# Kernel optimization log

Measured on AMD Instinct MI355X. Metric: run time of the kernel, lower is better.

Reference implementation:

```python
import jax, jax.numpy as jnp
import numpy as np

N_NODES = 50000
N_EDGES = 800000
D = 256


def setup_inputs() -> dict:
    key = jax.random.key(0)
    k1, k2, k3 = jax.random.split(key, 3)
    node_features = jax.random.normal(k1, (N_NODES, D), dtype=jnp.float32)
    edge_index = jax.random.randint(k2, (2, N_EDGES), 0, N_NODES, dtype=jnp.int64)
    # GCNConv linear weight (glorot-ish scale) and bias
    W = jax.random.normal(k3, (D, D), dtype=jnp.float32) * (1.0 / np.sqrt(D))
    b = jnp.zeros((D,), dtype=jnp.float32)
    alpha = jnp.full((1,), 0.5, dtype=jnp.float32)
    return {"node_features": node_features, "edge_index": edge_index, "W": W, "b": b, "alpha": alpha}


def _gcn_conv(x, edge_index, W, b):
    # PyG GCNConv: add self-loops, symmetric deg^{-1/2} normalization,
    # x' = W x, out[i] = sum_{j in N(i)} norm_ij * x'_j + b
    N = x.shape[0]
    loop = jnp.arange(N, dtype=edge_index.dtype)
    src = jnp.concatenate([edge_index[0], loop])  # [E+N]
    dst = jnp.concatenate([edge_index[1], loop])
    deg = jax.ops.segment_sum(jnp.ones(src.shape, dtype=x.dtype), dst, num_segments=N)
    dinv = jnp.where(deg > 0, jax.lax.rsqrt(jnp.maximum(deg, 1.0)), 0.0)
    norm = dinv[src] * dinv[dst]  # [E+N]
    h = x @ W.T  # [N, D]
    msg = h[src] * norm[:, None]  # gather + scale
    out = jax.ops.segment_sum(msg, dst, num_segments=N)  # scatter-add to targets
    return out + b


def reference(node_features, edge_index, W, b, alpha):
    updated = _gcn_conv(node_features, edge_index, W, b)
    a = alpha[0]
    # eval mode: dropout = identity; alpha-weighted residual blend
    return a * node_features + (1.0 - a) * updated
```

## Files before the change

### kernel.cpp

```cpp
#include <hip/hip_runtime.h>

#define N_NODES 50000
#define N_EDGES 800000
#define D 256
#define SLOT 64
#define GEMM_BLOCKS 391
#define FILL_BLOCKS 1563

typedef unsigned short bf16_t;
typedef __attribute__((ext_vector_type(8))) short short8;
typedef __attribute__((ext_vector_type(8))) unsigned short ushort8_t;
typedef __attribute__((ext_vector_type(4))) float f32x4;

__device__ inline float b2f(bf16_t u) {
    union { float f; unsigned v; } t; t.v = ((unsigned)u) << 16; return t.f;
}
__device__ inline bf16_t f2b(float f) {
    union { float f; unsigned v; } t; t.f = f;
    unsigned u = t.v;
    return (bf16_t)((u + 0x7FFFu + ((u >> 16) & 1u)) >> 16);
}
__device__ inline unsigned cvt_pk_bf16(float lo, float hi) {
    unsigned r;
    asm("v_cvt_pk_bf16_f32 %0, %1, %2" : "=v"(r) : "v"(lo), "v"(hi));
    return r;
}
__device__ inline short8 cvt8(float4 a, float4 b) {
    union { short8 s; unsigned u[4]; } t;
    t.u[0] = cvt_pk_bf16(a.x, a.y);
    t.u[1] = cvt_pk_bf16(a.z, a.w);
    t.u[2] = cvt_pk_bf16(b.x, b.y);
    t.u[3] = cvt_pk_bf16(b.z, b.w);
    return t.s;
}

__global__ void initcur_kernel(int* __restrict__ cursor) {
    int i = blockIdx.x * 256 + threadIdx.x;
    if (i < N_NODES) cursor[i] = i << 6;
}

__global__ __launch_bounds__(512) void k1_kernel(const float* __restrict__ x,
                                                 const float* __restrict__ W,
                                                 bf16_t* __restrict__ h,
                                                 const int* __restrict__ ei,
                                                 int* __restrict__ cursor,
                                                 int* __restrict__ csr_src) {
    __shared__ __align__(16) bf16_t As[128 * 32];
    __shared__ __align__(16) bf16_t Bs[256 * 32];

    const int tid = threadIdx.x;

    if (blockIdx.x >= GEMM_BLOCKS) {
        int e = (blockIdx.x - GEMM_BLOCKS) * 512 + tid;
        if (e < N_EDGES) {
            int s = ei[e];
            int d = ei[N_EDGES + e];
            if ((unsigned)d < (unsigned)N_NODES) {
                int pos = atomicAdd(&cursor[d], 1);
                csr_src[pos] = s;
            }
        }
        return;
    }

    const int wid  = tid >> 6;
    const int lane = tid & 63;
    const int wr = wid >> 2;
    const int wc = wid & 3;
    const int row0 = blockIdx.x * 128;
    const int lr = lane & 15;
    const int lk = (lane >> 4) * 8;

    const int srow = tid >> 2;
    const int sq   = tid & 3;
    int sr = row0 + srow;
    if (sr >= N_NODES) sr = N_NODES - 1;
    const float* agp = &x[(size_t)sr * D + sq * 8];
    bf16_t* alp = &As[srow * 32 + sq * 8];

    float4 areg[16];
#pragma unroll
    for (int s = 0; s < 8; s++) {
        const float4* p = reinterpret_cast<const float4*>(&agp[s * 32]);
        areg[2 * s]     = p[0];
        areg[2 * s + 1] = p[1];
    }

    f32x4 acc[4][4] = {};

#pragma unroll
    for (int s = 0; s < 8; s++) {
        *reinterpret_cast<short8*>(alp) = cvt8(areg[2 * s], areg[2 * s + 1]);
#pragma unroll
        for (int j = 0; j < 2; j++) {
            int brow = (j * 512 + tid) >> 2;
            const float4* q = reinterpret_cast<const float4*>(&W[(size_t)brow * D + s * 32 + sq * 8]);
            float4 w0 = q[0], w1 = q[1];
            *reinterpret_cast<short8*>(&Bs[brow * 32 + sq * 8]) = cvt8(w0, w1);
        }
        __syncthreads();

        short8 a[4], b[4];
#pragma unroll
        for (int m = 0; m < 4; m++)
            a[m] = *reinterpret_cast<const short8*>(&As[(wr * 64 + m * 16 + lr) * 32 + lk]);
#pragma unroll
        for (int n = 0; n < 4; n++)
            b[n] = *reinterpret_cast<const short8*>(&Bs[(wc * 64 + n * 16 + lr) * 32 + lk]);
#pragma unroll
        for (int m = 0; m < 4; m++)
#pragma unroll
            for (int n = 0; n < 4; n++)
                acc[m][n] = __builtin_amdgcn_mfma_f32_16x16x32_bf16(a[m], b[n], acc[m][n], 0, 0, 0);
        __syncthreads();
    }

#pragma unroll
    for (int m = 0; m < 4; m++) {
        int rbase = row0 + wr * 64 + m * 16 + (lane >> 4) * 4;
#pragma unroll
        for (int j = 0; j < 4; j++) {
            int rr = rbase + j;
            if (rr < N_NODES) {
#pragma unroll
                for (int n = 0; n < 4; n++)
                    h[(size_t)rr * D + wc * 64 + n * 16 + lr] = f2b(acc[m][n][j]);
            }
        }
    }
}

__global__ void dinv_kernel(const int* __restrict__ cursor, float* __restrict__ dinv) {
    int i = blockIdx.x * 256 + threadIdx.x;
    if (i < N_NODES) {
        int cnt = cursor[i] - (i << 6);
        dinv[i] = rsqrtf((float)(cnt + 1));
    }
}

__global__ __launch_bounds__(256) void gather_kernel(const int* __restrict__ cursor,
                                                     const int* __restrict__ csr_src,
                                                     const float* __restrict__ dinv,
                                                     const bf16_t* __restrict__ h,
                                                     const float* __restrict__ x,
                                                     const float* __restrict__ b,
                                                     const float* __restrict__ alpha,
                                                     float* __restrict__ out) {
    const int half = (threadIdx.x >> 5) & 1;
    const int wv   = threadIdx.x >> 6;
    const int ln   = threadIdx.x & 31;
    const int n = blockIdx.x * 8 + wv * 2 + half;
    if (n >= N_NODES) return;
    const int col = ln * 8;

    const int beg = n << 6;
    const int end = cursor[n];
    const float dn = dinv[n];
    const bf16_t* hl = h + col;

    float a0 = 0.f, a1 = 0.f, a2 = 0.f, a3 = 0.f,
          a4 = 0.f, a5 = 0.f, a6 = 0.f, a7 = 0.f;
    int k = beg;
    for (; k + 3 < end; k += 4) {
        int s0 = csr_src[k], s1 = csr_src[k + 1], s2 = csr_src[k + 2], s3 = csr_src[k + 3];
        float n0 = dinv[s0] * dn, n1 = dinv[s1] * dn, n2 = dinv[s2] * dn, n3 = dinv[s3] * dn;
        ushort8_t r0 = *reinterpret_cast<const ushort8_t*>(&hl[(size_t)s0 * D]);
        ushort8_t r1 = *reinterpret_cast<const ushort8_t*>(&hl[(size_t)s1 * D]);
        ushort8_t r2 = *reinterpret_cast<const ushort8_t*>(&hl[(size_t)s2 * D]);
        ushort8_t r3 = *reinterpret_cast<const ushort8_t*>(&hl[(size_t)s3 * D]);
        a0 += b2f(r0[0]) * n0 + b2f(r1[0]) * n1 + b2f(r2[0]) * n2 + b2f(r3[0]) * n3;
        a1 += b2f(r0[1]) * n0 + b2f(r1[1]) * n1 + b2f(r2[1]) * n2 + b2f(r3[1]) * n3;
        a2 += b2f(r0[2]) * n0 + b2f(r1[2]) * n1 + b2f(r2[2]) * n2 + b2f(r3[2]) * n3;
        a3 += b2f(r0[3]) * n0 + b2f(r1[3]) * n1 + b2f(r2[3]) * n2 + b2f(r3[3]) * n3;
        a4 += b2f(r0[4]) * n0 + b2f(r1[4]) * n1 + b2f(r2[4]) * n2 + b2f(r3[4]) * n3;
        a5 += b2f(r0[5]) * n0 + b2f(r1[5]) * n1 + b2f(r2[5]) * n2 + b2f(r3[5]) * n3;
        a6 += b2f(r0[6]) * n0 + b2f(r1[6]) * n1 + b2f(r2[6]) * n2 + b2f(r3[6]) * n3;
        a7 += b2f(r0[7]) * n0 + b2f(r1[7]) * n1 + b2f(r2[7]) * n2 + b2f(r3[7]) * n3;
    }
    for (; k < end; k++) {
        int s0 = csr_src[k];
        float n0 = dinv[s0] * dn;
        ushort8_t r0 = *reinterpret_cast<const ushort8_t*>(&hl[(size_t)s0 * D]);
        a0 += b2f(r0[0]) * n0; a1 += b2f(r0[1]) * n0;
        a2 += b2f(r0[2]) * n0; a3 += b2f(r0[3]) * n0;
        a4 += b2f(r0[4]) * n0; a5 += b2f(r0[5]) * n0;
        a6 += b2f(r0[6]) * n0; a7 += b2f(r0[7]) * n0;
    }

    const float dv2 = dn * dn;
    const float a   = alpha[0];
    ushort8_t hv = *reinterpret_cast<const ushort8_t*>(&hl[(size_t)n * D]);
    const float4* xp = reinterpret_cast<const float4*>(&x[(size_t)n * D + col]);
    const float4* bp = reinterpret_cast<const float4*>(&b[col]);
    float4 xv0 = xp[0], xv1 = xp[1];
    float4 bv0 = bp[0], bv1 = bp[1];
    float4 r0, r1;
    r0.x = a * xv0.x + (1.0f - a) * (a0 + dv2 * b2f(hv[0]) + bv0.x);
    r0.y = a * xv0.y + (1.0f - a) * (a1 + dv2 * b2f(hv[1]) + bv0.y);
    r0.z = a * xv0.z + (1.0f - a) * (a2 + dv2 * b2f(hv[2]) + bv0.z);
    r0.w = a * xv0.w + (1.0f - a) * (a3 + dv2 * b2f(hv[3]) + bv0.w);
    r1.x = a * xv1.x + (1.0f - a) * (a4 + dv2 * b2f(hv[4]) + bv1.x);
    r1.y = a * xv1.y + (1.0f - a) * (a5 + dv2 * b2f(hv[5]) + bv1.y);
    r1.z = a * xv1.z + (1.0f - a) * (a6 + dv2 * b2f(hv[6]) + bv1.z);
    r1.w = a * xv1.w + (1.0f - a) * (a7 + dv2 * b2f(hv[7]) + bv1.w);
    float4* op = reinterpret_cast<float4*>(&out[(size_t)n * D + col]);
    op[0] = r0;
    op[1] = r1;
}

extern "C" void kernel_launch(void* const* d_in, const int* in_sizes, int n_in,
                              void* d_out, int out_size, void* d_ws, size_t ws_size,
                              hipStream_t stream) {
    const float* x     = (const float*)d_in[0];
    const int*   ei    = (const int*)d_in[1];
    const float* W     = (const float*)d_in[2];
    const float* b     = (const float*)d_in[3];
    const float* alpha = (const float*)d_in[4];
    float* out = (float*)d_out;

    char* ws = (char*)d_ws;
    const size_t HB = (size_t)N_NODES * D * 2;
    bf16_t* h      = (bf16_t*)ws;
    int*   cursor  = (int*)  (ws + HB);
    float* dinv    = (float*)(ws + HB + 200000);
    int*   csr_src = (int*)  (ws + HB + 400000);

    initcur_kernel<<<(N_NODES + 255) / 256, 256, 0, stream>>>(cursor);
    k1_kernel<<<GEMM_BLOCKS + FILL_BLOCKS, 512, 0, stream>>>(x, W, h, ei, cursor, csr_src);
    dinv_kernel<<<(N_NODES + 255) / 256, 256, 0, stream>>>(cursor, dinv);
    gather_kernel<<<(N_NODES + 7) / 8, 256, 0, stream>>>(cursor, csr_src, dinv, h, x, b, alpha, out);
}
```

Measured before the change: 157.2 us.

## Stage full W in swizzled LDS, double-buffer A, fold CSR fill into GEMM blocks

The GEMM kernel now converts and stores all of W into LDS once, in an XOR-swizzled layout, instead of reloading a 32-wide slice on every k-step. The A tile is double-buffered, so each k-step needs one barrier instead of two. The separate edge-fill blocks are removed: each GEMM block handles 2048 edges of the CSR scatter while its x loads are in flight. The trade-off is about 144KB of LDS per block, which limits each CU to one block and leaves less latency hiding for the 391 blocks.

After: 140.9 us. -10.4%, faster.

```diff
diff --git a/kernel.cpp b/kernel.cpp
--- a/kernel.cpp
+++ b/kernel.cpp
@@ -5,7 +5,6 @@
 #define D 256
 #define SLOT 64
 #define GEMM_BLOCKS 391
-#define FILL_BLOCKS 1563
 
 typedef unsigned short bf16_t;
 typedef __attribute__((ext_vector_type(8))) short short8;
@@ -45,39 +44,17 @@
                                                  const int* __restrict__ ei,
                                                  int* __restrict__ cursor,
                                                  int* __restrict__ csr_src) {
-    __shared__ __align__(16) bf16_t As[128 * 32];
-    __shared__ __align__(16) bf16_t Bs[256 * 32];
+    __shared__ __align__(16) bf16_t Bs[256 * 256];
+    __shared__ __align__(16) bf16_t As[2 * 128 * 32];
 
     const int tid = threadIdx.x;
-
-    if (blockIdx.x >= GEMM_BLOCKS) {
-        int e = (blockIdx.x - GEMM_BLOCKS) * 512 + tid;
-        if (e < N_EDGES) {
-            int s = ei[e];
-            int d = ei[N_EDGES + e];
-            if ((unsigned)d < (unsigned)N_NODES) {
-                int pos = atomicAdd(&cursor[d], 1);
-                csr_src[pos] = s;
-            }
-        }
-        return;
-    }
-
-    const int wid  = tid >> 6;
-    const int lane = tid & 63;
-    const int wr = wid >> 2;
-    const int wc = wid & 3;
     const int row0 = blockIdx.x * 128;
-    const int lr = lane & 15;
-    const int lk = (lane >> 4) * 8;
 
     const int srow = tid >> 2;
     const int sq   = tid & 3;
     int sr = row0 + srow;
     if (sr >= N_NODES) sr = N_NODES - 1;
     const float* agp = &x[(size_t)sr * D + sq * 8];
-    bf16_t* alp = &As[srow * 32 + sq * 8];
-
     float4 areg[16];
 #pragma unroll
     for (int s = 0; s < 8; s++) {
@@ -86,38 +63,79 @@
         areg[2 * s + 1] = p[1];
     }
 
+    {
+        int e0 = blockIdx.x * 2048 + tid;
+        int ss[4], pos[4];
+        bool ok[4];
+#pragma unroll
+        for (int j = 0; j < 4; j++) {
+            int e = e0 + j * 512;
+            ok[j] = (e < N_EDGES);
+            int s = 0, d = 0;
+            if (ok[j]) { s = ei[e]; d = ei[N_EDGES + e]; }
+            ss[j] = s;
+            if (ok[j] && (unsigned)d < (unsigned)N_NODES)
+                pos[j] = atomicAdd(&cursor[d], 1);
+            else
+                ok[j] = false;
+        }
+#pragma unroll
+        for (int j = 0; j < 4; j++)
+            if (ok[j]) csr_src[pos[j]] = ss[j];
+    }
+
+#pragma unroll
+    for (int it = 0; it < 16; it++) {
+        int idx = it * 512 + tid;
+        int col = idx >> 5;
+        int c   = idx & 31;
+        const float4* q = reinterpret_cast<const float4*>(&W[(size_t)col * D + c * 8]);
+        short8 wv = cvt8(q[0], q[1]);
+        int phys = c ^ (col & 7);
+        *reinterpret_cast<short8*>(&Bs[col * 256 + (phys << 3)]) = wv;
+    }
+    __syncthreads();
+
+    const int wid  = tid >> 6;
+    const int lane = tid & 63;
+    const int wr = wid >> 2;
+    const int wc = wid & 3;
+    const int lr = lane & 15;
+    const int g  = lane >> 4;
+
     f32x4 acc[4][4] = {};
 
 #pragma unroll
     for (int s = 0; s < 8; s++) {
-        *reinterpret_cast<short8*>(alp) = cvt8(areg[2 * s], areg[2 * s + 1]);
-#pragma unroll
-        for (int j = 0; j < 2; j++) {
-            int brow = (j * 512 + tid) >> 2;
-            const float4* q = reinterpret_cast<const float4*>(&W[(size_t)brow * D + s * 32 + sq * 8]);
-            float4 w0 = q[0], w1 = q[1];
-            *reinterpret_cast<short8*>(&Bs[brow * 32 + sq * 8]) = cvt8(w0, w1);
-        }
+        *reinterpret_cast<short8*>(
+            &As[(s & 1) * 4096 + srow * 32 + ((sq ^ (srow & 3)) << 3)]) =
+            cvt8(areg[2 * s], areg[2 * s + 1]);
         __syncthreads();
 
         short8 a[4], b[4];
 #pragma unroll
-        for (int m = 0; m < 4; m++)
-            a[m] = *reinterpret_cast<const short8*>(&As[(wr * 64 + m * 16 + lr) * 32 + lk]);
-#pragma unroll
-        for (int n = 0; n < 4; n++)
-            b[n] = *reinterpret_cast<const short8*>(&Bs[(wc * 64 + n * 16 + lr) * 32 + lk]);
+        for (int m = 0; m < 4; m++) {
+            int row = wr * 64 + m * 16 + lr;
+            a[m] = *reinterpret_cast<const short8*>(
+                &As[(s & 1) * 4096 + row * 32 + ((g ^ (row & 3)) << 3)]);
+        }
+#pragma unroll
+        for (int n = 0; n < 4; n++) {
+            int col = wc * 64 + n * 16 + lr;
+            int c   = s * 4 + g;
+            int phys = c ^ (col & 7);
+            b[n] = *reinterpret_cast<const short8*>(&Bs[col * 256 + (phys << 3)]);
+        }
 #pragma unroll
         for (int m = 0; m < 4; m++)
 #pragma unroll
             for (int n = 0; n < 4; n++)
                 acc[m][n] = __builtin_amdgcn_mfma_f32_16x16x32_bf16(a[m], b[n], acc[m][n], 0, 0, 0);
-        __syncthreads();
     }
 
 #pragma unroll
     for (int m = 0; m < 4; m++) {
-        int rbase = row0 + wr * 64 + m * 16 + (lane >> 4) * 4;
+        int rbase = row0 + wr * 64 + m * 16 + g * 4;
 #pragma unroll
         for (int j = 0; j < 4; j++) {
             int rr = rbase + j;
@@ -226,7 +244,7 @@
     int*   csr_src = (int*)  (ws + HB + 400000);
 
     initcur_kernel<<<(N_NODES + 255) / 256, 256, 0, stream>>>(cursor);
-    k1_kernel<<<GEMM_BLOCKS + FILL_BLOCKS, 512, 0, stream>>>(x, W, h, ei, cursor, csr_src);
+    k1_kernel<<<GEMM_BLOCKS, 512, 0, stream>>>(x, W, h, ei, cursor, csr_src);
     dinv_kernel<<<(N_NODES + 255) / 256, 256, 0, stream>>>(cursor, dinv);
     gather_kernel<<<(N_NODES + 7) / 8, 256, 0, stream>>>(cursor, csr_src, dinv, h, x, b, alpha, out);
 }
```

## Aggregate raw bf16 features first, then fuse the GEMM into the gather kernel

Applied to the files above, without the earlier changes.

Uses linearity to reorder the computation as (A·x)·Wᵀ instead of A·(x·Wᵀ). Node features are converted to bf16 in a prep kernel, gathered and normalized per node, staged in shared memory, then multiplied by bf16 W with MFMA inside the same kernel before the residual blend. This removes the separate GEMM pass and its intermediate h write and read. In exchange, every block re-reads all of W from global or cache, the aggregated sums are rounded to bf16 before the matmul, and the edge-fill work now shares a launch with the conversion work.

After: 166.3 us. 5.8% more time.

```diff
diff --git a/kernel.cpp b/kernel.cpp
--- a/kernel.cpp
+++ b/kernel.cpp
@@ -4,8 +4,10 @@
 #define N_EDGES 800000
 #define D 256
 #define SLOT 64
-#define GEMM_BLOCKS 391
-#define FILL_BLOCKS 1563
+#define PADK 280
+#define FILL_BLOCKS 196
+#define CVTX_BLOCKS 3125
+#define CVTW_BLOCKS 16
 
 typedef unsigned short bf16_t;
 typedef __attribute__((ext_vector_type(8))) short short8;
@@ -14,11 +16,6 @@
 
 __device__ inline float b2f(bf16_t u) {
     union { float f; unsigned v; } t; t.v = ((unsigned)u) << 16; return t.f;
-}
-__device__ inline bf16_t f2b(float f) {
-    union { float f; unsigned v; } t; t.f = f;
-    unsigned u = t.v;
-    return (bf16_t)((u + 0x7FFFu + ((u >> 16) & 1u)) >> 16);
 }
 __device__ inline unsigned cvt_pk_bf16(float lo, float hi) {
     unsigned r;
@@ -39,94 +36,40 @@
     if (i < N_NODES) cursor[i] = i << 6;
 }
 
-__global__ __launch_bounds__(512) void k1_kernel(const float* __restrict__ x,
-                                                 const float* __restrict__ W,
-                                                 bf16_t* __restrict__ h,
-                                                 const int* __restrict__ ei,
-                                                 int* __restrict__ cursor,
-                                                 int* __restrict__ csr_src) {
-    __shared__ __align__(16) bf16_t As[128 * 32];
-    __shared__ __align__(16) bf16_t Bs[256 * 32];
-
+__global__ __launch_bounds__(512) void prep_kernel(const float* __restrict__ x,
+                                                   const float* __restrict__ W,
+                                                   const int* __restrict__ ei,
+                                                   int* __restrict__ cursor,
+                                                   int* __restrict__ csr_src,
+                                                   bf16_t* __restrict__ xb,
+                                                   bf16_t* __restrict__ Wb) {
     const int tid = threadIdx.x;
-
-    if (blockIdx.x >= GEMM_BLOCKS) {
-        int e = (blockIdx.x - GEMM_BLOCKS) * 512 + tid;
-        if (e < N_EDGES) {
-            int s = ei[e];
-            int d = ei[N_EDGES + e];
-            if ((unsigned)d < (unsigned)N_NODES) {
-                int pos = atomicAdd(&cursor[d], 1);
-                csr_src[pos] = s;
+    const int bid = blockIdx.x;
+
+    if (bid < FILL_BLOCKS) {
+        int e0 = bid * 4096 + tid;
+#pragma unroll
+        for (int j = 0; j < 8; j++) {
+            int e = e0 + j * 512;
+            if (e < N_EDGES) {
+                int s = ei[e];
+                int d = ei[N_EDGES + e];
+                if ((unsigned)d < (unsigned)N_NODES) {
+                    int pos = atomicAdd(&cursor[d], 1);
+                    csr_src[pos] = s;
+                }
             }
         }
-        return;
-    }
-
-    const int wid  = tid >> 6;
-    const int lane = tid & 63;
-    const int wr = wid >> 2;
-    const int wc = wid & 3;
-    const int row0 = blockIdx.x * 128;
-    const int lr = lane & 15;
-    const int lk = (lane >> 4) * 8;
-
-    const int srow = tid >> 2;
-    const int sq   = tid & 3;
-    int sr = row0 + srow;
-    if (sr >= N_NODES) sr = N_NODES - 1;
-    const float* agp = &x[(size_t)sr * D + sq * 8];
-    bf16_t* alp = &As[srow * 32 + sq * 8];
-
-    float4 areg[16];
-#pragma unroll
-    for (int s = 0; s < 8; s++) {
-        const float4* p = reinterpret_cast<const float4*>(&agp[s * 32]);
-        areg[2 * s]     = p[0];
-        areg[2 * s + 1] = p[1];
-    }
-
-    f32x4 acc[4][4] = {};
-
-#pragma unroll
-    for (int s = 0; s < 8; s++) {
-        *reinterpret_cast<short8*>(alp) = cvt8(areg[2 * s], areg[2 * s + 1]);
-#pragma unroll
-        for (int j = 0; j < 2; j++) {
-            int brow = (j * 512 + tid) >> 2;
-            const float4* q = reinterpret_cast<const float4*>(&W[(size_t)brow * D + s * 32 + sq * 8]);
-            float4 w0 = q[0], w1 = q[1];
-            *reinterpret_cast<short8*>(&Bs[brow * 32 + sq * 8]) = cvt8(w0, w1);
-        }
-        __syncthreads();
-
-        short8 a[4], b[4];
-#pragma unroll
-        for (int m = 0; m < 4; m++)
-            a[m] = *reinterpret_cast<const short8*>(&As[(wr * 64 + m * 16 + lr) * 32 + lk]);
-#pragma unroll
-        for (int n = 0; n < 4; n++)
-            b[n] = *reinterpret_cast<const short8*>(&Bs[(wc * 64 + n * 16 + lr) * 32 + lk]);
-#pragma unroll
-        for (int m = 0; m < 4; m++)
-#pragma unroll
-            for (int n = 0; n < 4; n++)
-                acc[m][n] = __builtin_amdgcn_mfma_f32_16x16x32_bf16(a[m], b[n], acc[m][n], 0, 0, 0);
-        __syncthreads();
-    }
-
-#pragma unroll
-    for (int m = 0; m < 4; m++) {
-        int rbase = row0 + wr * 64 + m * 16 + (lane >> 4) * 4;
-#pragma unroll
-        for (int j = 0; j < 4; j++) {
-            int rr = rbase + j;
-            if (rr < N_NODES) {
-#pragma unroll
-                for (int n = 0; n < 4; n++)
-                    h[(size_t)rr * D + wc * 64 + n * 16 + lr] = f2b(acc[m][n][j]);
-            }
-        }
+    } else if (bid < FILL_BLOCKS + CVTX_BLOCKS) {
+        int i = (bid - FILL_BLOCKS) * 512 + tid;
+        const float4* p = reinterpret_cast<const float4*>(x) + (size_t)i * 2;
+        float4 v0 = p[0], v1 = p[1];
+        *reinterpret_cast<short8*>(&xb[(size_t)i * 8]) = cvt8(v0, v1);
+    } else {
+        int i = (bid - FILL_BLOCKS - CVTX_BLOCKS) * 512 + tid;
+        const float4* p = reinterpret_cast<const float4*>(W) + (size_t)i * 2;
+        float4 v0 = p[0], v1 = p[1];
+        *reinterpret_cast<short8*>(&Wb[(size_t)i * 8]) = cvt8(v0, v1);
     }
 }
 
@@ -138,74 +81,102 @@
     }
 }
 
-__global__ __launch_bounds__(256) void gather_kernel(const int* __restrict__ cursor,
-                                                     const int* __restrict__ csr_src,
-                                                     const float* __restrict__ dinv,
-                                                     const bf16_t* __restrict__ h,
-                                                     const float* __restrict__ x,
-                                                     const float* __restrict__ b,
-                                                     const float* __restrict__ alpha,
-                                                     float* __restrict__ out) {
-    const int half = (threadIdx.x >> 5) & 1;
-    const int wv   = threadIdx.x >> 6;
-    const int ln   = threadIdx.x & 31;
-    const int n = blockIdx.x * 8 + wv * 2 + half;
-    if (n >= N_NODES) return;
+__global__ __launch_bounds__(512) void gather_gemm_kernel(const int* __restrict__ cursor,
+                                                          const int* __restrict__ csr_src,
+                                                          const float* __restrict__ dinv,
+                                                          const bf16_t* __restrict__ xb,
+                                                          const bf16_t* __restrict__ Wb,
+                                                          const float* __restrict__ x,
+                                                          const float* __restrict__ b,
+                                                          const float* __restrict__ alpha,
+                                                          float* __restrict__ out) {
+    __shared__ __align__(16) bf16_t As[16 * PADK];
+
+    const int tid = threadIdx.x;
+    const int r   = tid >> 5;
+    const int ln  = tid & 31;
+    const int n   = blockIdx.x * 16 + r;
     const int col = ln * 8;
 
-    const int beg = n << 6;
-    const int end = cursor[n];
-    const float dn = dinv[n];
-    const bf16_t* hl = h + col;
-
-    float a0 = 0.f, a1 = 0.f, a2 = 0.f, a3 = 0.f,
-          a4 = 0.f, a5 = 0.f, a6 = 0.f, a7 = 0.f;
-    int k = beg;
-    for (; k + 3 < end; k += 4) {
-        int s0 = csr_src[k], s1 = csr_src[k + 1], s2 = csr_src[k + 2], s3 = csr_src[k + 3];
-        float n0 = dinv[s0] * dn, n1 = dinv[s1] * dn, n2 = dinv[s2] * dn, n3 = dinv[s3] * dn;
-        ushort8_t r0 = *reinterpret_cast<const ushort8_t*>(&hl[(size_t)s0 * D]);
-        ushort8_t r1 = *reinterpret_cast<const ushort8_t*>(&hl[(size_t)s1 * D]);
-        ushort8_t r2 = *reinterpret_cast<const ushort8_t*>(&hl[(size_t)s2 * D]);
-        ushort8_t r3 = *reinterpret_cast<const ushort8_t*>(&hl[(size_t)s3 * D]);
-        a0 += b2f(r0[0]) * n0 + b2f(r1[0]) * n1 + b2f(r2[0]) * n2 + b2f(r3[0]) * n3;
-        a1 += b2f(r0[1]) * n0 + b2f(r1[1]) * n1 + b2f(r2[1]) * n2 + b2f(r3[1]) * n3;
-        a2 += b2f(r0[2]) * n0 + b2f(r1[2]) * n1 + b2f(r2[2]) * n2 + b2f(r3[2]) * n3;
-        a3 += b2f(r0[3]) * n0 + b2f(r1[3]) * n1 + b2f(r2[3]) * n2 + b2f(r3[3]) * n3;
-        a4 += b2f(r0[4]) * n0 + b2f(r1[4]) * n1 + b2f(r2[4]) * n2 + b2f(r3[4]) * n3;
-        a5 += b2f(r0[5]) * n0 + b2f(r1[5]) * n1 + b2f(r2[5]) * n2 + b2f(r3[5]) * n3;
-        a6 += b2f(r0[6]) * n0 + b2f(r1[6]) * n1 + b2f(r2[6]) * n2 + b2f(r3[6]) * n3;
-        a7 += b2f(r0[7]) * n0 + b2f(r1[7]) * n1 + b2f(r2[7]) * n2 + b2f(r3[7]) * n3;
-    }
-    for (; k < end; k++) {
-        int s0 = csr_src[k];
-        float n0 = dinv[s0] * dn;
-        ushort8_t r0 = *reinterpret_cast<const ushort8_t*>(&hl[(size_t)s0 * D]);
-        a0 += b2f(r0[0]) * n0; a1 += b2f(r0[1]) * n0;
-        a2 += b2f(r0[2]) * n0; a3 += b2f(r0[3]) * n0;
-        a4 += b2f(r0[4]) * n0; a5 += b2f(r0[5]) * n0;
-        a6 += b2f(r0[6]) * n0; a7 += b2f(r0[7]) * n0;
-    }
-
-    const float dv2 = dn * dn;
-    const float a   = alpha[0];
-    ushort8_t hv = *reinterpret_cast<const ushort8_t*>(&hl[(size_t)n * D]);
-    const float4* xp = reinterpret_cast<const float4*>(&x[(size_t)n * D + col]);
-    const float4* bp = reinterpret_cast<const float4*>(&b[col]);
-    float4 xv0 = xp[0], xv1 = xp[1];
-    float4 bv0 = bp[0], bv1 = bp[1];
-    float4 r0, r1;
-    r0.x = a * xv0.x + (1.0f - a) * (a0 + dv2 * b2f(hv[0]) + bv0.x);
-    r0.y = a * xv0.y + (1.0f - a) * (a1 + dv2 * b2f(hv[1]) + bv0.y);
-    r0.z = a * xv0.z + (1.0f - a) * (a2 + dv2 * b2f(hv[2]) + bv0.z);
-    r0.w = a * xv0.w + (1.0f - a) * (a3 + dv2 * b2f(hv[3]) + bv0.w);
-    r1.x = a * xv1.x + (1.0f - a) * (a4 + dv2 * b2f(hv[4]) + bv1.x);
-    r1.y = a * xv1.y + (1.0f - a) * (a5 + dv2 * b2f(hv[5]) + bv1.y);
-    r1.z = a * xv1.z + (1.0f - a) * (a6 + dv2 * b2f(hv[6]) + bv1.z);
-    r1.w = a * xv1.w + (1.0f - a) * (a7 + dv2 * b2f(hv[7]) + bv1.w);
-    float4* op = reinterpret_cast<float4*>(&out[(size_t)n * D + col]);
-    op[0] = r0;
-    op[1] = r1;
+    {
+        const int beg = n << 6;
+        const int end = cursor[n];
+        const float dn = dinv[n];
+        const bf16_t* hl = xb + col;
+
+        float a0 = 0.f, a1 = 0.f, a2 = 0.f, a3 = 0.f,
+              a4 = 0.f, a5 = 0.f, a6 = 0.f, a7 = 0.f;
+        int k = beg;
+        for (; k + 3 < end; k += 4) {
+            int s0 = csr_src[k], s1 = csr_src[k + 1], s2 = csr_src[k + 2], s3 = csr_src[k + 3];
+            float n0 = dinv[s0] * dn, n1 = dinv[s1] * dn, n2 = dinv[s2] * dn, n3 = dinv[s3] * dn;
+            ushort8_t r0 = *reinterpret_cast<const ushort8_t*>(&hl[(size_t)s0 * D]);
+            ushort8_t r1 = *reinterpret_cast<const ushort8_t*>(&hl[(size_t)s1 * D]);
+            ushort8_t r2 = *reinterpret_cast<const ushort8_t*>(&hl[(size_t)s2 * D]);
+            ushort8_t r3 = *reinterpret_cast<const ushort8_t*>(&hl[(size_t)s3 * D]);
+            a0 += b2f(r0[0]) * n0 + b2f(r1[0]) * n1 + b2f(r2[0]) * n2 + b2f(r3[0]) * n3;
+            a1 += b2f(r0[1]) * n0 + b2f(r1[1]) * n1 + b2f(r2[1]) * n2 + b2f(r3[1]) * n3;
+            a2 += b2f(r0[2]) * n0 + b2f(r1[2]) * n1 + b2f(r2[2]) * n2 + b2f(r3[2]) * n3;
+            a3 += b2f(r0[3]) * n0 + b2f(r1[3]) * n1 + b2f(r2[3]) * n2 + b2f(r3[3]) * n3;
+            a4 += b2f(r0[4]) * n0 + b2f(r1[4]) * n1 + b2f(r2[4]) * n2 + b2f(r3[4]) * n3;
+            a5 += b2f(r0[5]) * n0 + b2f(r1[5]) * n1 + b2f(r2[5]) * n2 + b2f(r3[5]) * n3;
+            a6 += b2f(r0[6]) * n0 + b2f(r1[6]) * n1 + b2f(r2[6]) * n2 + b2f(r3[6]) * n3;
+            a7 += b2f(r0[7]) * n0 + b2f(r1[7]) * n1 + b2f(r2[7]) * n2 + b2f(r3[7]) * n3;
+        }
+        for (; k < end; k++) {
+            int s0 = csr_src[k];
+            float n0 = dinv[s0] * dn;
+            ushort8_t r0 = *reinterpret_cast<const ushort8_t*>(&hl[(size_t)s0 * D]);
+            a0 += b2f(r0[0]) * n0; a1 += b2f(r0[1]) * n0;
+            a2 += b2f(r0[2]) * n0; a3 += b2f(r0[3]) * n0;
+            a4 += b2f(r0[4]) * n0; a5 += b2f(r0[5]) * n0;
+            a6 += b2f(r0[6]) * n0; a7 += b2f(r0[7]) * n0;
+        }
+        const float dv2 = dn * dn;
+        ushort8_t hv = *reinterpret_cast<const ushort8_t*>(&hl[(size_t)n * D]);
+        a0 += dv2 * b2f(hv[0]); a1 += dv2 * b2f(hv[1]);
+        a2 += dv2 * b2f(hv[2]); a3 += dv2 * b2f(hv[3]);
+        a4 += dv2 * b2f(hv[4]); a5 += dv2 * b2f(hv[5]);
+        a6 += dv2 * b2f(hv[6]); a7 += dv2 * b2f(hv[7]);
+
+        union { short8 s; unsigned u[4]; } t;
+        t.u[0] = cvt_pk_bf16(a0, a1);
+        t.u[1] = cvt_pk_bf16(a2, a3);
+        t.u[2] = cvt_pk_bf16(a4, a5);
+        t.u[3] = cvt_pk_bf16(a6, a7);
+        *reinterpret_cast<short8*>(&As[r * PADK + col]) = t.s;
+    }
+    __syncthreads();
+
+    const int w    = tid >> 6;
+    const int lane = tid & 63;
+    const int lr = lane & 15;
+    const int g  = lane >> 4;
+
+    f32x4 acc0 = {}, acc1 = {};
+    const bf16_t* wp0 = &Wb[(size_t)(w * 32 + lr) * D];
+    const bf16_t* wp1 = &Wb[(size_t)(w * 32 + 16 + lr) * D];
+#pragma unroll
+    for (int ks = 0; ks < 8; ks++) {
+        short8 a = *reinterpret_cast<const short8*>(&As[lr * PADK + ks * 32 + g * 8]);
+        short8 b0 = *reinterpret_cast<const short8*>(&wp0[ks * 32 + g * 8]);
+        short8 b1 = *reinterpret_cast<const short8*>(&wp1[ks * 32 + g * 8]);
+        acc0 = __builtin_amdgcn_mfma_f32_16x16x32_bf16(a, b0, acc0, 0, 0, 0);
+        acc1 = __builtin_amdgcn_mfma_f32_16x16x32_bf16(a, b1, acc1, 0, 0, 0);
+    }
+
+    const float av = alpha[0];
+    const int c0 = w * 32 + lr;
+    const int c1 = c0 + 16;
+    const float b0v = b[c0];
+    const float b1v = b[c1];
+#pragma unroll
+    for (int j = 0; j < 4; j++) {
+        int node = blockIdx.x * 16 + g * 4 + j;
+        size_t base = (size_t)node * D;
+        out[base + c0] = av * x[base + c0] + (1.0f - av) * (acc0[j] + b0v);
+        out[base + c1] = av * x[base + c1] + (1.0f - av) * (acc1[j] + b1v);
+    }
 }
 
 extern "C" void kernel_launch(void* const* d_in, const int* in_sizes, int n_in,
@@ -219,14 +190,17 @@
     float* out = (float*)d_out;
 
     char* ws = (char*)d_ws;
-    const size_t HB = (size_t)N_NODES * D * 2;
-    bf16_t* h      = (bf16_t*)ws;
-    int*   cursor  = (int*)  (ws + HB);
-    float* dinv    = (float*)(ws + HB + 200000);
-    int*   csr_src = (int*)  (ws + HB + 400000);
+    const size_t XB = (size_t)N_NODES * D * 2;
+    bf16_t* xb     = (bf16_t*)ws;
+    bf16_t* Wb     = (bf16_t*)(ws + XB);
+    int*   cursor  = (int*)  (ws + XB + 131072);
+    float* dinv    = (float*)(ws + XB + 331072);
+    int*   csr_src = (int*)  (ws + XB + 531072);
 
     initcur_kernel<<<(N_NODES + 255) / 256, 256, 0, stream>>>(cursor);
-    k1_kernel<<<GEMM_BLOCKS + FILL_BLOCKS, 512, 0, stream>>>(x, W, h, ei, cursor, csr_src);
+    prep_kernel<<<FILL_BLOCKS + CVTX_BLOCKS + CVTW_BLOCKS, 512, 0, stream>>>(
+        x, W, ei, cursor, csr_src, xb, Wb);
     dinv_kernel<<<(N_NODES + 255) / 256, 256, 0, stream>>>(cursor, dinv);
-    gather_kernel<<<(N_NODES + 7) / 8, 256, 0, stream>>>(cursor, csr_src, dinv, h, x, b, alpha, out);
-}
+    gather_gemm_kernel<<<N_NODES / 16, 512, 0, stream>>>(
+        cursor, csr_src, dinv, xb, Wb, x, b, alpha, out);
+}
```

## Use 8-way striped CSR slots with sentinel padding and precast W to bf16

Applied to the files above, without the earlier changes.

Each node's adjacency slot grows to 128 entries and is split into 8 interleaved cursors chosen by edge index. This spreads atomic contention across sub-counters, and the gather can read rows of 8 source indices with int4 loads. Unused slots are pre-filled with a sentinel node whose h row and dinv are zero, so the gather loop runs a branch-free 8-wide unrolled body up to the longest stripe. W is converted to bf16 once in an init kernel rather than by every GEMM block, and fill blocks each process 8 edges. In exchange the init kernel writes a 25.6 MB sentinel buffer, and the gather wastes reads whenever stripes are uneven.

Result: slower. 164.0 us (+4.3%).

```diff
diff --git a/kernel.cpp b/kernel.cpp
--- a/kernel.cpp
+++ b/kernel.cpp
@@ -3,9 +3,12 @@
 #define N_NODES 50000
 #define N_EDGES 800000
 #define D 256
-#define SLOT 64
+#define SLOT 128
 #define GEMM_BLOCKS 391
-#define FILL_BLOCKS 1563
+#define FILL_BLOCKS 196
+#define CUR_INIT_BLOCKS 1563
+#define SENT_BLOCKS 6250
+#define WCVT_BLOCKS 32
 
 typedef unsigned short bf16_t;
 typedef __attribute__((ext_vector_type(8))) short short8;
@@ -34,13 +37,42 @@
     return t.s;
 }
 
-__global__ void initcur_kernel(int* __restrict__ cursor) {
-    int i = blockIdx.x * 256 + threadIdx.x;
-    if (i < N_NODES) cursor[i] = i << 6;
+__global__ __launch_bounds__(256) void init_kernel(const float* __restrict__ W,
+                                                   int* __restrict__ cursor,
+                                                   int* __restrict__ csr_src,
+                                                   bf16_t* __restrict__ h,
+                                                   bf16_t* __restrict__ Wb) {
+    const int tid = threadIdx.x;
+    int bid = blockIdx.x;
+
+    if (bid < CUR_INIT_BLOCKS) {
+        int i = bid * 256 + tid;
+        if (i < N_NODES * 8) cursor[i] = ((i >> 3) << 7) | (i & 7);
+        return;
+    }
+    bid -= CUR_INIT_BLOCKS;
+    if (bid < SENT_BLOCKS) {
+        int i = bid * 256 + tid;
+        int4 v = make_int4(N_NODES, N_NODES, N_NODES, N_NODES);
+        reinterpret_cast<int4*>(csr_src)[i] = v;
+        return;
+    }
+    bid -= SENT_BLOCKS;
+    if (bid == 0) {
+        if (tid < 128) reinterpret_cast<int*>(&h[(size_t)N_NODES * D])[tid] = 0;
+        return;
+    }
+    bid -= 1;
+    {
+        int i = (bid * 256 + tid);
+        const float4* p = reinterpret_cast<const float4*>(W) + (size_t)i * 2;
+        float4 v0 = p[0], v1 = p[1];
+        *reinterpret_cast<short8*>(&Wb[(size_t)i * 8]) = cvt8(v0, v1);
+    }
 }
 
 __global__ __launch_bounds__(512) void k1_kernel(const float* __restrict__ x,
-                                                 const float* __restrict__ W,
+                                                 const bf16_t* __restrict__ Wb,
                                                  bf16_t* __restrict__ h,
                                                  const int* __restrict__ ei,
                                                  int* __restrict__ cursor,
@@ -51,13 +83,17 @@
     const int tid = threadIdx.x;
 
     if (blockIdx.x >= GEMM_BLOCKS) {
-        int e = (blockIdx.x - GEMM_BLOCKS) * 512 + tid;
-        if (e < N_EDGES) {
-            int s = ei[e];
-            int d = ei[N_EDGES + e];
-            if ((unsigned)d < (unsigned)N_NODES) {
-                int pos = atomicAdd(&cursor[d], 1);
-                csr_src[pos] = s;
+        int e0 = (blockIdx.x - GEMM_BLOCKS) * 4096 + tid;
+#pragma unroll
+        for (int j = 0; j < 8; j++) {
+            int e = e0 + j * 512;
+            if (e < N_EDGES) {
+                int s = ei[e];
+                int d = ei[N_EDGES + e];
+                if ((unsigned)d < (unsigned)N_NODES) {
+                    int pos = atomicAdd(&cursor[d * 8 + (e & 7)], 8);
+                    csr_src[pos] = s;
+                }
             }
         }
         return;
@@ -94,9 +130,8 @@
 #pragma unroll
         for (int j = 0; j < 2; j++) {
             int brow = (j * 512 + tid) >> 2;
-            const float4* q = reinterpret_cast<const float4*>(&W[(size_t)brow * D + s * 32 + sq * 8]);
-            float4 w0 = q[0], w1 = q[1];
-            *reinterpret_cast<short8*>(&Bs[brow * 32 + sq * 8]) = cvt8(w0, w1);
+            short8 wv = *reinterpret_cast<const short8*>(&Wb[(size_t)brow * D + s * 32 + sq * 8]);
+            *reinterpret_cast<short8*>(&Bs[brow * 32 + sq * 8]) = wv;
         }
         __syncthreads();
 
@@ -132,10 +167,14 @@
 
 __global__ void dinv_kernel(const int* __restrict__ cursor, float* __restrict__ dinv) {
     int i = blockIdx.x * 256 + threadIdx.x;
-    if (i < N_NODES) {
-        int cnt = cursor[i] - (i << 6);
-        dinv[i] = rsqrtf((float)(cnt + 1));
-    }
+    if (i > N_NODES) return;
+    if (i == N_NODES) { dinv[i] = 0.0f; return; }
+    const int4* cp = reinterpret_cast<const int4*>(&cursor[i * 8]);
+    int4 c0 = cp[0], c1 = cp[1];
+    int base = i << 7;
+    int cnt = ((c0.x - base) + (c0.y - base - 1) + (c0.z - base - 2) + (c0.w - base - 3)
+             + (c1.x - base - 4) + (c1.y - base - 5) + (c1.z - base - 6) + (c1.w - base - 7)) >> 3;
+    dinv[i] = rsqrtf((float)(cnt + 1));
 }
 
 __global__ __launch_bounds__(256) void gather_kernel(const int* __restrict__ cursor,
@@ -153,59 +192,70 @@
     if (n >= N_NODES) return;
     const int col = ln * 8;
 
-    const int beg = n << 6;
-    const int end = cursor[n];
+    const int4* cp = reinterpret_cast<const int4*>(&cursor[n * 8]);
+    int4 c0 = cp[0], c1 = cp[1];
+    const int base = n << 7;
+    int m0 = max(max(c0.x - 0, c0.y - 1), max(c0.z - 2, c0.w - 3));
+    int m1 = max(max(c1.x - 4, c1.y - 5), max(c1.z - 6, c1.w - 7));
+    const int maxc = (max(m0, m1) - base) >> 3;
+
     const float dn = dinv[n];
     const bf16_t* hl = h + col;
 
     float a0 = 0.f, a1 = 0.f, a2 = 0.f, a3 = 0.f,
           a4 = 0.f, a5 = 0.f, a6 = 0.f, a7 = 0.f;
-    int k = beg;
-    for (; k + 3 < end; k += 4) {
-        int s0 = csr_src[k], s1 = csr_src[k + 1], s2 = csr_src[k + 2], s3 = csr_src[k + 3];
-        float n0 = dinv[s0] * dn, n1 = dinv[s1] * dn, n2 = dinv[s2] * dn, n3 = dinv[s3] * dn;
-        ushort8_t r0 = *reinterpret_cast<const ushort8_t*>(&hl[(size_t)s0 * D]);
-        ushort8_t r1 = *reinterpret_cast<const ushort8_t*>(&hl[(size_t)s1 * D]);
-        ushort8_t r2 = *reinterpret_cast<const ushort8_t*>(&hl[(size_t)s2 * D]);
-        ushort8_t r3 = *reinterpret_cast<const ushort8_t*>(&hl[(size_t)s3 * D]);
-        a0 += b2f(r0[0]) * n0 + b2f(r1[0]) * n1 + b2f(r2[0]) * n2 + b2f(r3[0]) * n3;
-        a1 += b2f(r0[1]) * n0 + b2f(r1[1]) * n1 + b2f(r2[1]) * n2 + b2f(r3[1]) * n3;
-        a2 += b2f(r0[2]) * n0 + b2f(r1[2]) * n1 + b2f(r2[2]) * n2 + b2f(r3[2]) * n3;
-        a3 += b2f(r0[3]) * n0 + b2f(r1[3]) * n1 + b2f(r2[3]) * n2 + b2f(r3[3]) * n3;
-        a4 += b2f(r0[4]) * n0 + b2f(r1[4]) * n1 + b2f(r2[4]) * n2 + b2f(r3[4]) * n3;
-        a5 += b2f(r0[5]) * n0 + b2f(r1[5]) * n1 + b2f(r2[5]) * n2 + b2f(r3[5]) * n3;
-        a6 += b2f(r0[6]) * n0 + b2f(r1[6]) * n1 + b2f(r2[6]) * n2 + b2f(r3[6]) * n3;
-        a7 += b2f(r0[7]) * n0 + b2f(r1[7]) * n1 + b2f(r2[7]) * n2 + b2f(r3[7]) * n3;
-    }
-    for (; k < end; k++) {
-        int s0 = csr_src[k];
-        float n0 = dinv[s0] * dn;
-        ushort8_t r0 = *reinterpret_cast<const ushort8_t*>(&hl[(size_t)s0 * D]);
-        a0 += b2f(r0[0]) * n0; a1 += b2f(r0[1]) * n0;
-        a2 += b2f(r0[2]) * n0; a3 += b2f(r0[3]) * n0;
-        a4 += b2f(r0[4]) * n0; a5 += b2f(r0[5]) * n0;
-        a6 += b2f(r0[6]) * n0; a7 += b2f(r0[7]) * n0;
+    for (int r = 0; r < maxc; r++) {
+        const int4* sp = reinterpret_cast<const int4*>(&csr_src[base + r * 8]);
+        int4 u0 = sp[0], u1 = sp[1];
+        float n0 = dinv[u0.x] * dn, n1 = dinv[u0.y] * dn,
+              n2 = dinv[u0.z] * dn, n3 = dinv[u0.w] * dn;
+        float n4 = dinv[u1.x] * dn, n5 = dinv[u1.y] * dn,
+              n6 = dinv[u1.z] * dn, n7 = dinv[u1.w] * dn;
+        ushort8_t r0 = *reinterpret_cast<const ushort8_t*>(&hl[(size_t)u0.x * D]);
+        ushort8_t r1 = *reinterpret_cast<const ushort8_t*>(&hl[(size_t)u0.y * D]);
+        ushort8_t r2 = *reinterpret_cast<const ushort8_t*>(&hl[(size_t)u0.z * D]);
+        ushort8_t r3 = *reinterpret_cast<const ushort8_t*>(&hl[(size_t)u0.w * D]);
+        ushort8_t r4 = *reinterpret_cast<const ushort8_t*>(&hl[(size_t)u1.x * D]);
+        ushort8_t r5 = *reinterpret_cast<const ushort8_t*>(&hl[(size_t)u1.y * D]);
+        ushort8_t r6 = *reinterpret_cast<const ushort8_t*>(&hl[(size_t)u1.z * D]);
+        ushort8_t r7 = *reinterpret_cast<const ushort8_t*>(&hl[(size_t)u1.w * D]);
+        a0 += b2f(r0[0]) * n0 + b2f(r1[0]) * n1 + b2f(r2[0]) * n2 + b2f(r3[0]) * n3
+            + b2f(r4[0]) * n4 + b2f(r5[0]) * n5 + b2f(r6[0]) * n6 + b2f(r7[0]) * n7;
+        a1 += b2f(r0[1]) * n0 + b2f(r1[1]) * n1 + b2f(r2[1]) * n2 + b2f(r3[1]) * n3
+            + b2f(r4[1]) * n4 + b2f(r5[1]) * n5 + b2f(r6[1]) * n6 + b2f(r7[1]) * n7;
+        a2 += b2f(r0[2]) * n0 + b2f(r1[2]) * n1 + b2f(r2[2]) * n2 + b2f(r3[2]) * n3
+            + b2f(r4[2]) * n4 + b2f(r5[2]) * n5 + b2f(r6[2]) * n6 + b2f(r7[2]) * n7;
+        a3 += b2f(r0[3]) * n0 + b2f(r1[3]) * n1 + b2f(r2[3]) * n2 + b2f(r3[3]) * n3
+            + b2f(r4[3]) * n4 + b2f(r5[3]) * n5 + b2f(r6[3]) * n6 + b2f(r7[3]) * n7;
+        a4 += b2f(r0[4]) * n0 + b2f(r1[4]) * n1 + b2f(r2[4]) * n2 + b2f(r3[4]) * n3
+            + b2f(r4[4]) * n4 + b2f(r5[4]) * n5 + b2f(r6[4]) * n6 + b2f(r7[4]) * n7;
+        a5 += b2f(r0[5]) * n0 + b2f(r1[5]) * n1 + b2f(r2[5]) * n2 + b2f(r3[5]) * n3
+            + b2f(r4[5]) * n4 + b2f(r5[5]) * n5 + b2f(r6[5]) * n6 + b2f(r7[5]) * n7;
+        a6 += b2f(r0[6]) * n0 + b2f(r1[6]) * n1 + b2f(r2[6]) * n2 + b2f(r3[6]) * n3
+            + b2f(r4[6]) * n4 + b2f(r5[6]) * n5 + b2f(r6[6]) * n6 + b2f(r7[6]) * n7;
+        a7 += b2f(r0[7]) * n0 + b2f(r1[7]) * n1 + b2f(r2[7]) * n2 + b2f(r3[7]) * n3
+            + b2f(r4[7]) * n4 + b2f(r5[7]) * n5 + b2f(r6[7]) * n6 + b2f(r7[7]) * n7;
     }
 
     const float dv2 = dn * dn;
-    const float a   = alpha[0];
+    const float av  = alpha[0];
     ushort8_t hv = *reinterpret_cast<const ushort8_t*>(&hl[(size_t)n * D]);
     const float4* xp = reinterpret_cast<const float4*>(&x[(size_t)n * D + col]);
     const float4* bp = reinterpret_cast<const float4*>(&b[col]);
     float4 xv0 = xp[0], xv1 = xp[1];
     float4 bv0 = bp[0], bv1 = bp[1];
-    float4 r0, r1;
-    r0.x = a * xv0.x + (1.0f - a) * (a0 + dv2 * b2f(hv[0]) + bv0.x);
-    r0.y = a * xv0.y + (1.0f - a) * (a1 + dv2 * b2f(hv[1]) + bv0.y);
-    r0.z = a * xv0.z + (1.0f - a) * (a2 + dv2 * b2f(hv[2]) + bv0.z);
-    r0.w = a * xv0.w + (1.0f - a) * (a3 + dv2 * b2f(hv[3]) + bv0.w);
-    r1.x = a * xv1.x + (1.0f - a) * (a4 + dv2 * b2f(hv[4]) + bv1.x);
-    r1.y = a * xv1.y + (1.0f - a) * (a5 + dv2 * b2f(hv[5]) + bv1.y);
-    r1.z = a * xv1.z + (1.0f - a) * (a6 + dv2 * b2f(hv[6]) + bv1.z);
-    r1.w = a * xv1.w + (1.0f - a) * (a7 + dv2 * b2f(hv[7]) + bv1.w);
+    float4 o0, o1;
+    o0.x = av * xv0.x + (1.0f - av) * (a0 + dv2 * b2f(hv[0]) + bv0.x);
+    o0.y = av * xv0.y + (1.0f - av) * (a1 + dv2 * b2f(hv[1]) + bv0.y);
+    o0.z = av * xv0.z + (1.0f - av) * (a2 + dv2 * b2f(hv[2]) + bv0.z);
+    o0.w = av * xv0.w + (1.0f - av) * (a3 + dv2 * b2f(hv[3]) + bv0.w);
+    o1.x = av * xv1.x + (1.0f - av) * (a4 + dv2 * b2f(hv[4]) + bv1.x);
+    o1.y = av * xv1.y + (1.0f - av) * (a5 + dv2 * b2f(hv[5]) + bv1.y);
+    o1.z = av * xv1.z + (1.0f - av) * (a6 + dv2 * b2f(hv[6]) + bv1.z);
+    o1.w = av * xv1.w + (1.0f - av) * (a7 + dv2 * b2f(hv[7]) + bv1.w);
     float4* op = reinterpret_cast<float4*>(&out[(size_t)n * D + col]);
-    op[0] = r0;
-    op[1] = r1;
+    op[0] = o0;
+    op[1] = o1;
 }
 
 extern "C" void kernel_launch(void* const* d_in, const int* in_sizes, int n_in,
@@ -219,14 +269,16 @@
     float* out = (float*)d_out;
 
     char* ws = (char*)d_ws;
-    const size_t HB = (size_t)N_NODES * D * 2;
+    const size_t HB = (size_t)(N_NODES + 1) * D * 2;
     bf16_t* h      = (bf16_t*)ws;
-    int*   cursor  = (int*)  (ws + HB);
-    float* dinv    = (float*)(ws + HB + 200000);
-    int*   csr_src = (int*)  (ws + HB + 400000);
-
-    initcur_kernel<<<(N_NODES + 255) / 256, 256, 0, stream>>>(cursor);
-    k1_kernel<<<GEMM_BLOCKS + FILL_BLOCKS, 512, 0, stream>>>(x, W, h, ei, cursor, csr_src);
-    dinv_kernel<<<(N_NODES + 255) / 256, 256, 0, stream>>>(cursor, dinv);
+    bf16_t* Wb     = (bf16_t*)(ws + HB);
+    int*   cursor  = (int*)  (ws + HB + 131072);
+    float* dinv    = (float*)(ws + HB + 1731072);
+    int*   csr_src = (int*)  (ws + HB + 1931076 + 12);
+
+    init_kernel<<<CUR_INIT_BLOCKS + SENT_BLOCKS + 1 + WCVT_BLOCKS, 256, 0, stream>>>(
+        W, cursor, csr_src, h, Wb);
+    k1_kernel<<<GEMM_BLOCKS + FILL_BLOCKS, 512, 0, stream>>>(x, Wb, h, ei, cursor, csr_src);
+    dinv_kernel<<<(N_NODES + 256) / 256, 256, 0, stream>>>(cursor, dinv);
     gather_kernel<<<(N_NODES + 7) / 8, 256, 0, stream>>>(cursor, csr_src, dinv, h, x, b, alpha, out);
 }
```
